# Kernel optimization log

Hardware: AMD Instinct MI355X
Metric: run time of the kernel (lower is better)

Reference implementation:

```python
import jax, jax.numpy as jnp
import numpy as np

B, T, D = 2, 1024, 384
d = D // 3            # 128
D3 = 3 * d            # 384
D9 = 9 * d            # 1152
GAMMA = 5.0
EPS_W = 1e-8
EPS_N = 1e-5


def _orth(rng, n):
    q, _ = np.linalg.qr(rng.standard_normal((n, n)).astype(np.float64))
    return jnp.asarray(q.astype(np.float32))


def setup_inputs() -> dict:
    key = jax.random.key(0)
    x = jax.random.normal(key, (B, T, D), dtype=jnp.float32)
    rng = np.random.default_rng(0)
    def plin(fan_in, fan_out):
        W = jnp.asarray(rng.standard_normal((fan_out, fan_in)).astype(np.float32) * 0.05)
        b = jnp.zeros((fan_out,), jnp.float32)
        return W, b
    Wq, bq = plin(d, D3); Sq = _orth(rng, D3)
    Wk, bk = plin(d, D3); Sk = _orth(rng, D3)
    Wv, bv = plin(d, D3); Sv = _orth(rng, D3)
    Wp, bp = plin(D3, D9)
    gn = jnp.ones((D9,), jnp.float32)
    bn = jnp.zeros((D9,), jnp.float32)
    return {"x": x, "Wq": Wq, "bq": bq, "Sq": Sq, "Wk": Wk, "bk": bk, "Sk": Sk,
            "Wv": Wv, "bv": bv, "Sv": Sv, "Wp": Wp, "bp": bp, "gn": gn, "bn": bn}


def _plin(x, W, b):
    # PositiveLinearHK: linear with softplus-positive weights
    return x @ jax.nn.softplus(W).T + b


def reference(x, Wq, bq, Sq, Wk, bk, Sk, Wv, bv, Sv, Wp, bp, gn, bn):
    Q_base = x[:, :, 0 * d:1 * d]
    K_base = x[:, :, 1 * d:2 * d]
    V_base = x[:, :, 2 * d:3 * d]
    # proj = PositiveLinearHK -> SingleStiefelProjector (orthogonal mixing)
    Q = _plin(Q_base, Wq, bq) @ Sq          # (B,T,3d)
    K = _plin(K_base, Wk, bk) @ Sk
    V = _plin(V_base, Wv, bv) @ Sv
    dots = jnp.einsum('bti,btj->btij', Q, K)            # (B,T,3d,3d)
    scores = jax.nn.sigmoid(GAMMA * dots)
    weights = scores / (scores.sum(axis=-1, keepdims=True) + EPS_W)
    attended = jnp.einsum('btij,btj->bti', weights, V)  # (B,T,3d)
    h = _plin(attended, Wp, bp)                         # (B,T,9d)
    mu = h.mean(axis=-1, keepdims=True)
    var = h.var(axis=-1, keepdims=True)
    return (h - mu) * jax.lax.rsqrt(var + EPS_N) * gn + bn
```

## Files before the change

### kernel.cpp

```cpp
#include <hip/hip_runtime.h>
#include <hip/hip_bf16.h>
#include <math.h>

#define NTOK  2048
#define DD    128
#define DD3   384
#define DD9   1152
#define TB    4
#define GAMMA_F 5.0f
#define LN2_F   0.69314718f
#define LOG2E_F 1.44269504f

#define OFF_M    0
#define OFF_C    147456
#define OFF_WP2  148608

__device__ __forceinline__ float softplusf(float x) {
    return fmaxf(x, 0.0f) + log1pf(__expf(-fabsf(x)));
}
__device__ __forceinline__ unsigned short f2bf(float f) {
    __hip_bfloat16 h = __float2bfloat16(f);
    return *reinterpret_cast<unsigned short*>(&h);
}
__device__ __forceinline__ float exp2_fast(float x) {
#if __has_builtin(__builtin_amdgcn_exp2f)
    return __builtin_amdgcn_exp2f(x);
#else
    return __expf(x * LN2_F);
#endif
}

__global__ __launch_bounds__(384) void k_prep(const float* __restrict__ Wq, const float* __restrict__ Wk,
                                              const float* __restrict__ Wv, const float* __restrict__ Wp,
                                              const float* __restrict__ Sq, const float* __restrict__ Sk,
                                              const float* __restrict__ Sv, const float* __restrict__ bq,
                                              const float* __restrict__ bk, const float* __restrict__ bv,
                                              float* __restrict__ ws) {
    __shared__ float sw[DD3];
    int b = blockIdx.x, tid = threadIdx.x;
    if (b < 384) {
        int idx = b * 384 + tid;
        int i = idx / DD3, m = idx % DD3;
        unsigned d0 = f2bf(softplusf(Wp[(0 * DD3 + m) * DD3 + i]) - LN2_F);
        unsigned d1 = f2bf(softplusf(Wp[(1 * DD3 + m) * DD3 + i]) - LN2_F);
        unsigned d2 = f2bf(softplusf(Wp[(2 * DD3 + m) * DD3 + i]) - LN2_F);
        uint2 u; u.x = d0 | (d1 << 16); u.y = d2;
        ((uint2*)(ws + OFF_WP2))[idx] = u;
    } else if (b < 768) {
        int bb = b - 384;
        int mat = bb >> 7, i = bb & 127;
        const float* W = (mat == 0) ? Wq : (mat == 1 ? Wk : Wv);
        const float* S = (mat == 0) ? Sq : (mat == 1 ? Sk : Sv);
        int m = tid;
        sw[m] = softplusf(W[m * DD + i]);
        __syncthreads();
        const float4* sw4 = (const float4*)sw;
        float a0 = 0.f, a1 = 0.f, a2 = 0.f, a3 = 0.f;
        for (int j4 = 0; j4 < 96; ++j4) {
            float4 w = sw4[j4];
            int j = j4 * 4;
            a0 = fmaf(w.x, S[(j + 0) * DD3 + m], a0);
            a1 = fmaf(w.y, S[(j + 1) * DD3 + m], a1);
            a2 = fmaf(w.z, S[(j + 2) * DD3 + m], a2);
            a3 = fmaf(w.w, S[(j + 3) * DD3 + m], a3);
        }
        ws[OFF_M + mat * 49152 + i * DD3 + m] = (a0 + a1) + (a2 + a3);
    } else {
        int mat = b - 768;
        const float* S = (mat == 0) ? Sq : (mat == 1 ? Sk : Sv);
        const float* bb_ = (mat == 0) ? bq : (mat == 1 ? bk : bv);
        int m = tid;
        float a0 = 0.f, a1 = 0.f, a2 = 0.f, a3 = 0.f;
        for (int j4 = 0; j4 < 96; ++j4) {
            int j = j4 * 4;
            a0 = fmaf(bb_[j + 0], S[(j + 0) * DD3 + m], a0);
            a1 = fmaf(bb_[j + 1], S[(j + 1) * DD3 + m], a1);
            a2 = fmaf(bb_[j + 2], S[(j + 2) * DD3 + m], a2);
            a3 = fmaf(bb_[j + 3], S[(j + 3) * DD3 + m], a3);
        }
        ws[OFF_C + mat * DD3 + m] = (a0 + a1) + (a2 + a3);
    }
}

#define SIGROW(NQ, RS, AV) do {                                        \
        float e0 = exp2_fast((NQ) * kk.x);                             \
        float e1 = exp2_fast((NQ) * kk.y);                             \
        float e2 = exp2_fast((NQ) * kk.z);                             \
        float e3 = exp2_fast((NQ) * kk.w);                             \
        float s0 = __builtin_amdgcn_rcpf(1.0f + e0);                   \
        float s1 = __builtin_amdgcn_rcpf(1.0f + e1);                   \
        float s2 = __builtin_amdgcn_rcpf(1.0f + e2);                   \
        float s3 = __builtin_amdgcn_rcpf(1.0f + e3);                   \
        RS += (s0 + s1) + (s2 + s3);                                   \
        AV = fmaf(s0, vv.x, fmaf(s1, vv.y, fmaf(s2, vv.z, fmaf(s3, vv.w, AV)))); \
    } while (0)

__global__ __launch_bounds__(384, 3) void k_fused(const float* __restrict__ x,
                                                  const float* __restrict__ bp,
                                                  const float* __restrict__ gn,
                                                  const float* __restrict__ bn,
                                                  const float* __restrict__ ws,
                                                  float* __restrict__ out) {
    __shared__ float qkv[3 * TB * DD3];
    __shared__ float att[TB * DD3];
    __shared__ float red[32];
    __shared__ float ssum[TB], smu[TB], sinv[TB];

    int tid = threadIdx.x;
    int tok0 = blockIdx.x * TB;
    const float* xb = x + (size_t)tok0 * DD3;

#pragma unroll
    for (int mat = 0; mat < 3; ++mat) {
        const float* M = ws + OFF_M + mat * 49152;
        const float* xt0 = xb + 0 * DD3 + mat * DD;
        const float* xt1 = xb + 1 * DD3 + mat * DD;
        const float* xt2 = xb + 2 * DD3 + mat * DD;
        const float* xt3 = xb + 3 * DD3 + mat * DD;
        float a0 = 0.f, a1 = 0.f, a2 = 0.f, a3 = 0.f;
        for (int i = 0; i < DD; i += 4) {
            float m0 = M[(i + 0) * DD3 + tid];
            float m1 = M[(i + 1) * DD3 + tid];
            float m2 = M[(i + 2) * DD3 + tid];
            float m3 = M[(i + 3) * DD3 + tid];
            a0 = fmaf(xt0[i], m0, fmaf(xt0[i + 1], m1, fmaf(xt0[i + 2], m2, fmaf(xt0[i + 3], m3, a0))));
            a1 = fmaf(xt1[i], m0, fmaf(xt1[i + 1], m1, fmaf(xt1[i + 2], m2, fmaf(xt1[i + 3], m3, a1))));
            a2 = fmaf(xt2[i], m0, fmaf(xt2[i + 1], m1, fmaf(xt2[i + 2], m2, fmaf(xt2[i + 3], m3, a2))));
            a3 = fmaf(xt3[i], m0, fmaf(xt3[i + 1], m1, fmaf(xt3[i + 2], m2, fmaf(xt3[i + 3], m3, a3))));
        }
        float c = ws[OFF_C + mat * DD3 + tid];
        qkv[(mat * TB + 0) * DD3 + tid] = a0 + c;
        qkv[(mat * TB + 1) * DD3 + tid] = a1 + c;
        qkv[(mat * TB + 2) * DD3 + tid] = a2 + c;
        qkv[(mat * TB + 3) * DD3 + tid] = a3 + c;
    }
    __syncthreads();

    {
        int t  = tid / 96;
        int ts = tid - t * 96;
        const float* Qt = qkv + t * DD3;
        float nq0 = Qt[ts +   0] * (-GAMMA_F * LOG2E_F);
        float nq1 = Qt[ts +  96] * (-GAMMA_F * LOG2E_F);
        float nq2 = Qt[ts + 192] * (-GAMMA_F * LOG2E_F);
        float nq3 = Qt[ts + 288] * (-GAMMA_F * LOG2E_F);
        const float4* K4 = (const float4*)(qkv + (TB + t) * DD3);
        const float4* V4 = (const float4*)(qkv + (2 * TB + t) * DD3);
        float rs0 = 0.f, rs1 = 0.f, rs2 = 0.f, rs3 = 0.f;
        float av0 = 0.f, av1 = 0.f, av2 = 0.f, av3 = 0.f;
        for (int j4 = 0; j4 < 96; ++j4) {
            float4 kk = K4[j4];
            float4 vv = V4[j4];
            SIGROW(nq0, rs0, av0);
            SIGROW(nq1, rs1, av1);
            SIGROW(nq2, rs2, av2);
            SIGROW(nq3, rs3, av3);
        }
        att[t * DD3 + ts +   0] = av0 * __builtin_amdgcn_rcpf(rs0 + 1e-8f);
        att[t * DD3 + ts +  96] = av1 * __builtin_amdgcn_rcpf(rs1 + 1e-8f);
        att[t * DD3 + ts + 192] = av2 * __builtin_amdgcn_rcpf(rs2 + 1e-8f);
        att[t * DD3 + ts + 288] = av3 * __builtin_amdgcn_rcpf(rs3 + 1e-8f);
    }
    __syncthreads();

    int wave = tid >> 6, lane = tid & 63;

    {
        float s0 = att[0 * DD3 + tid];
        float s1 = att[1 * DD3 + tid];
        float s2 = att[2 * DD3 + tid];
        float s3 = att[3 * DD3 + tid];
#pragma unroll
        for (int off = 32; off; off >>= 1) {
            s0 += __shfl_down(s0, off, 64);
            s1 += __shfl_down(s1, off, 64);
            s2 += __shfl_down(s2, off, 64);
            s3 += __shfl_down(s3, off, 64);
        }
        if (lane == 0) {
            red[0 * 8 + wave] = s0; red[1 * 8 + wave] = s1;
            red[2 * 8 + wave] = s2; red[3 * 8 + wave] = s3;
        }
        __syncthreads();
        if (tid < TB) {
            float a = 0.f;
            for (int w = 0; w < 6; ++w) a += red[tid * 8 + w];
            ssum[tid] = a;
        }
        __syncthreads();
    }

    const uint2* wp2 = (const uint2*)(ws + OFF_WP2);
    float acc[3][TB];
    {
        float bp0 = bp[tid], bp1 = bp[tid + DD3], bp2 = bp[tid + 2 * DD3];
#pragma unroll
        for (int t = 0; t < TB; ++t) {
            float base = LN2_F * ssum[t];
            acc[0][t] = bp0 + base;
            acc[1][t] = bp1 + base;
            acc[2][t] = bp2 + base;
        }
    }
    const float4* att4 = (const float4*)att;
    for (int i4 = 0; i4 < 96; ++i4) {
        float4 a0 = att4[0 * 96 + i4];
        float4 a1 = att4[1 * 96 + i4];
        float4 a2 = att4[2 * 96 + i4];
        float4 a3 = att4[3 * 96 + i4];
        const float* af0 = (const float*)&a0;
        const float* af1 = (const float*)&a1;
        const float* af2 = (const float*)&a2;
        const float* af3 = (const float*)&a3;
#pragma unroll
        for (int e = 0; e < 4; ++e) {
            uint2 u = wp2[(i4 * 4 + e) * DD3 + tid];
            float w0 = __uint_as_float(u.x << 16);
            float w1 = __uint_as_float(u.x & 0xffff0000u);
            float w2 = __uint_as_float(u.y << 16);
            acc[0][0] = fmaf(af0[e], w0, acc[0][0]);
            acc[1][0] = fmaf(af0[e], w1, acc[1][0]);
            acc[2][0] = fmaf(af0[e], w2, acc[2][0]);
            acc[0][1] = fmaf(af1[e], w0, acc[0][1]);
            acc[1][1] = fmaf(af1[e], w1, acc[1][1]);
            acc[2][1] = fmaf(af1[e], w2, acc[2][1]);
            acc[0][2] = fmaf(af2[e], w0, acc[0][2]);
            acc[1][2] = fmaf(af2[e], w1, acc[1][2]);
            acc[2][2] = fmaf(af2[e], w2, acc[2][2]);
            acc[0][3] = fmaf(af3[e], w0, acc[0][3]);
            acc[1][3] = fmaf(af3[e], w1, acc[1][3]);
            acc[2][3] = fmaf(af3[e], w2, acc[2][3]);
        }
    }

#pragma unroll
    for (int t = 0; t < TB; ++t) {
        float s = acc[0][t] + acc[1][t] + acc[2][t];
#pragma unroll
        for (int off = 32; off; off >>= 1) s += __shfl_down(s, off, 64);
        if (lane == 0) red[t * 8 + wave] = s;
    }
    __syncthreads();
    if (tid < TB) {
        float a = 0.f;
        for (int w = 0; w < 6; ++w) a += red[tid * 8 + w];
        smu[tid] = a * (1.0f / 1152.0f);
    }
    __syncthreads();
#pragma unroll
    for (int t = 0; t < TB; ++t) {
        float mu = smu[t];
        acc[0][t] -= mu; acc[1][t] -= mu; acc[2][t] -= mu;
        float s = fmaf(acc[0][t], acc[0][t], fmaf(acc[1][t], acc[1][t], acc[2][t] * acc[2][t]));
#pragma unroll
        for (int off = 32; off; off >>= 1) s += __shfl_down(s, off, 64);
        if (lane == 0) red[t * 8 + wave] = s;
    }
    __syncthreads();
    if (tid < TB) {
        float b = 0.f;
        for (int w = 0; w < 6; ++w) b += red[tid * 8 + w];
        sinv[tid] = __builtin_amdgcn_rsqf(b * (1.0f / 1152.0f) + 1e-5f);
    }
    __syncthreads();
    float g0 = gn[tid], g1 = gn[tid + DD3], g2 = gn[tid + 2 * DD3];
    float b0 = bn[tid], b1 = bn[tid + DD3], b2 = bn[tid + 2 * DD3];
#pragma unroll
    for (int t = 0; t < TB; ++t) {
        float inv = sinv[t];
        size_t base = (size_t)(tok0 + t) * DD9;
        out[base + tid]           = fmaf(acc[0][t] * inv, g0, b0);
        out[base + tid + DD3]     = fmaf(acc[1][t] * inv, g1, b1);
        out[base + tid + 2 * DD3] = fmaf(acc[2][t] * inv, g2, b2);
    }
}

extern "C" void kernel_launch(void* const* d_in, const int* in_sizes, int n_in,
                              void* d_out, int out_size, void* d_ws, size_t ws_size,
                              hipStream_t stream) {
    const float* x  = (const float*)d_in[0];
    const float* Wq = (const float*)d_in[1];
    const float* bq = (const float*)d_in[2];
    const float* Sq = (const float*)d_in[3];
    const float* Wk = (const float*)d_in[4];
    const float* bk = (const float*)d_in[5];
    const float* Sk = (const float*)d_in[6];
    const float* Wv = (const float*)d_in[7];
    const float* bv = (const float*)d_in[8];
    const float* Sv = (const float*)d_in[9];
    const float* Wp = (const float*)d_in[10];
    const float* bp = (const float*)d_in[11];
    const float* gn = (const float*)d_in[12];
    const float* bn = (const float*)d_in[13];
    float* out = (float*)d_out;
    float* ws  = (float*)d_ws;

    hipLaunchKernelGGL(k_prep, dim3(771), dim3(384), 0, stream,
                       Wq, Wk, Wv, Wp, Sq, Sk, Sv, bq, bk, bv, ws);
    hipLaunchKernelGGL(k_fused, dim3(NTOK / TB), dim3(384), 0, stream, x, bp, gn, bn, ws, out);
}
```

Before: 159.4 us.

## Halve tokens per block to two, double occupancy, use packed FMA

Cuts tokens per block from four to two, which doubles the grid to 1024 blocks, and raises the launch-bounds occupancy hint from 3 to 6. The attention stage is remapped so each thread handles two query rows instead of four. The output projection now accumulates with 2-wide vector FMAs that can map to packed fp32 FMA. The aim is more blocks to fill the CUs and better latency hiding, at the cost of half the reuse of each projection weight loaded from global memory, so weight traffic doubles.

```diff
diff --git a/kernel.cpp b/kernel.cpp
--- a/kernel.cpp
+++ b/kernel.cpp
@@ -6,7 +6,7 @@
 #define DD    128
 #define DD3   384
 #define DD9   1152
-#define TB    4
+#define TB    2
 #define GAMMA_F 5.0f
 #define LN2_F   0.69314718f
 #define LOG2E_F 1.44269504f
@@ -14,6 +14,8 @@
 #define OFF_M    0
 #define OFF_C    147456
 #define OFF_WP2  148608
+
+typedef __attribute__((ext_vector_type(2))) float f32x2;
 
 __device__ __forceinline__ float softplusf(float x) {
     return fmaxf(x, 0.0f) + log1pf(__expf(-fabsf(x)));
@@ -95,7 +97,7 @@
         AV = fmaf(s0, vv.x, fmaf(s1, vv.y, fmaf(s2, vv.z, fmaf(s3, vv.w, AV)))); \
     } while (0)
 
-__global__ __launch_bounds__(384, 3) void k_fused(const float* __restrict__ x,
+__global__ __launch_bounds__(384, 6) void k_fused(const float* __restrict__ x,
                                                   const float* __restrict__ bp,
                                                   const float* __restrict__ gn,
                                                   const float* __restrict__ bn,
@@ -103,7 +105,7 @@
                                                   float* __restrict__ out) {
     __shared__ float qkv[3 * TB * DD3];
     __shared__ float att[TB * DD3];
-    __shared__ float red[32];
+    __shared__ float red[16];
     __shared__ float ssum[TB], smu[TB], sinv[TB];
 
     int tid = threadIdx.x;
@@ -115,9 +117,7 @@
         const float* M = ws + OFF_M + mat * 49152;
         const float* xt0 = xb + 0 * DD3 + mat * DD;
         const float* xt1 = xb + 1 * DD3 + mat * DD;
-        const float* xt2 = xb + 2 * DD3 + mat * DD;
-        const float* xt3 = xb + 3 * DD3 + mat * DD;
-        float a0 = 0.f, a1 = 0.f, a2 = 0.f, a3 = 0.f;
+        float a0 = 0.f, a1 = 0.f;
         for (int i = 0; i < DD; i += 4) {
             float m0 = M[(i + 0) * DD3 + tid];
             float m1 = M[(i + 1) * DD3 + tid];
@@ -125,62 +125,44 @@
             float m3 = M[(i + 3) * DD3 + tid];
             a0 = fmaf(xt0[i], m0, fmaf(xt0[i + 1], m1, fmaf(xt0[i + 2], m2, fmaf(xt0[i + 3], m3, a0))));
             a1 = fmaf(xt1[i], m0, fmaf(xt1[i + 1], m1, fmaf(xt1[i + 2], m2, fmaf(xt1[i + 3], m3, a1))));
-            a2 = fmaf(xt2[i], m0, fmaf(xt2[i + 1], m1, fmaf(xt2[i + 2], m2, fmaf(xt2[i + 3], m3, a2))));
-            a3 = fmaf(xt3[i], m0, fmaf(xt3[i + 1], m1, fmaf(xt3[i + 2], m2, fmaf(xt3[i + 3], m3, a3))));
         }
         float c = ws[OFF_C + mat * DD3 + tid];
         qkv[(mat * TB + 0) * DD3 + tid] = a0 + c;
         qkv[(mat * TB + 1) * DD3 + tid] = a1 + c;
-        qkv[(mat * TB + 2) * DD3 + tid] = a2 + c;
-        qkv[(mat * TB + 3) * DD3 + tid] = a3 + c;
     }
     __syncthreads();
 
     {
-        int t  = tid / 96;
-        int ts = tid - t * 96;
+        int t  = tid / 192;
+        int ts = tid - t * 192;
         const float* Qt = qkv + t * DD3;
-        float nq0 = Qt[ts +   0] * (-GAMMA_F * LOG2E_F);
-        float nq1 = Qt[ts +  96] * (-GAMMA_F * LOG2E_F);
-        float nq2 = Qt[ts + 192] * (-GAMMA_F * LOG2E_F);
-        float nq3 = Qt[ts + 288] * (-GAMMA_F * LOG2E_F);
+        float nq0 = Qt[ts]       * (-GAMMA_F * LOG2E_F);
+        float nq1 = Qt[ts + 192] * (-GAMMA_F * LOG2E_F);
         const float4* K4 = (const float4*)(qkv + (TB + t) * DD3);
         const float4* V4 = (const float4*)(qkv + (2 * TB + t) * DD3);
-        float rs0 = 0.f, rs1 = 0.f, rs2 = 0.f, rs3 = 0.f;
-        float av0 = 0.f, av1 = 0.f, av2 = 0.f, av3 = 0.f;
+        float rs0 = 0.f, rs1 = 0.f, av0 = 0.f, av1 = 0.f;
         for (int j4 = 0; j4 < 96; ++j4) {
             float4 kk = K4[j4];
             float4 vv = V4[j4];
             SIGROW(nq0, rs0, av0);
             SIGROW(nq1, rs1, av1);
-            SIGROW(nq2, rs2, av2);
-            SIGROW(nq3, rs3, av3);
-        }
-        att[t * DD3 + ts +   0] = av0 * __builtin_amdgcn_rcpf(rs0 + 1e-8f);
-        att[t * DD3 + ts +  96] = av1 * __builtin_amdgcn_rcpf(rs1 + 1e-8f);
-        att[t * DD3 + ts + 192] = av2 * __builtin_amdgcn_rcpf(rs2 + 1e-8f);
-        att[t * DD3 + ts + 288] = av3 * __builtin_amdgcn_rcpf(rs3 + 1e-8f);
-    }
-    __syncthreads();
-
-    int wave = tid >> 6, lane = tid & 63;
+        }
+        att[t * DD3 + ts]       = av0 * __builtin_amdgcn_rcpf(rs0 + 1e-8f);
+        att[t * DD3 + ts + 192] = av1 * __builtin_amdgcn_rcpf(rs1 + 1e-8f);
+    }
+    __syncthreads();
+
+    int wave = tid >> 6, lane64 = tid & 63;
 
     {
         float s0 = att[0 * DD3 + tid];
         float s1 = att[1 * DD3 + tid];
-        float s2 = att[2 * DD3 + tid];
-        float s3 = att[3 * DD3 + tid];
 #pragma unroll
         for (int off = 32; off; off >>= 1) {
             s0 += __shfl_down(s0, off, 64);
             s1 += __shfl_down(s1, off, 64);
-            s2 += __shfl_down(s2, off, 64);
-            s3 += __shfl_down(s3, off, 64);
-        }
-        if (lane == 0) {
-            red[0 * 8 + wave] = s0; red[1 * 8 + wave] = s1;
-            red[2 * 8 + wave] = s2; red[3 * 8 + wave] = s3;
-        }
+        }
+        if (lane64 == 0) { red[wave] = s0; red[8 + wave] = s1; }
         __syncthreads();
         if (tid < TB) {
             float a = 0.f;
@@ -191,54 +173,40 @@
     }
 
     const uint2* wp2 = (const uint2*)(ws + OFF_WP2);
-    float acc[3][TB];
+    f32x2 acc2[3];
     {
         float bp0 = bp[tid], bp1 = bp[tid + DD3], bp2 = bp[tid + 2 * DD3];
-#pragma unroll
-        for (int t = 0; t < TB; ++t) {
-            float base = LN2_F * ssum[t];
-            acc[0][t] = bp0 + base;
-            acc[1][t] = bp1 + base;
-            acc[2][t] = bp2 + base;
-        }
+        float b0 = LN2_F * ssum[0], b1 = LN2_F * ssum[1];
+        acc2[0] = (f32x2){bp0 + b0, bp0 + b1};
+        acc2[1] = (f32x2){bp1 + b0, bp1 + b1};
+        acc2[2] = (f32x2){bp2 + b0, bp2 + b1};
     }
     const float4* att4 = (const float4*)att;
     for (int i4 = 0; i4 < 96; ++i4) {
         float4 a0 = att4[0 * 96 + i4];
         float4 a1 = att4[1 * 96 + i4];
-        float4 a2 = att4[2 * 96 + i4];
-        float4 a3 = att4[3 * 96 + i4];
         const float* af0 = (const float*)&a0;
         const float* af1 = (const float*)&a1;
-        const float* af2 = (const float*)&a2;
-        const float* af3 = (const float*)&a3;
 #pragma unroll
         for (int e = 0; e < 4; ++e) {
             uint2 u = wp2[(i4 * 4 + e) * DD3 + tid];
             float w0 = __uint_as_float(u.x << 16);
             float w1 = __uint_as_float(u.x & 0xffff0000u);
             float w2 = __uint_as_float(u.y << 16);
-            acc[0][0] = fmaf(af0[e], w0, acc[0][0]);
-            acc[1][0] = fmaf(af0[e], w1, acc[1][0]);
-            acc[2][0] = fmaf(af0[e], w2, acc[2][0]);
-            acc[0][1] = fmaf(af1[e], w0, acc[0][1]);
-            acc[1][1] = fmaf(af1[e], w1, acc[1][1]);
-            acc[2][1] = fmaf(af1[e], w2, acc[2][1]);
-            acc[0][2] = fmaf(af2[e], w0, acc[0][2]);
-            acc[1][2] = fmaf(af2[e], w1, acc[1][2]);
-            acc[2][2] = fmaf(af2[e], w2, acc[2][2]);
-            acc[0][3] = fmaf(af3[e], w0, acc[0][3]);
-            acc[1][3] = fmaf(af3[e], w1, acc[1][3]);
-            acc[2][3] = fmaf(af3[e], w2, acc[2][3]);
-        }
-    }
+            f32x2 a01 = (f32x2){af0[e], af1[e]};
+            acc2[0] = __builtin_elementwise_fma(a01, (f32x2){w0, w0}, acc2[0]);
+            acc2[1] = __builtin_elementwise_fma(a01, (f32x2){w1, w1}, acc2[1]);
+            acc2[2] = __builtin_elementwise_fma(a01, (f32x2){w2, w2}, acc2[2]);
+        }
+    }
+    float av_[3][TB] = {{acc2[0].x, acc2[0].y}, {acc2[1].x, acc2[1].y}, {acc2[2].x, acc2[2].y}};
 
 #pragma unroll
     for (int t = 0; t < TB; ++t) {
-        float s = acc[0][t] + acc[1][t] + acc[2][t];
+        float s = av_[0][t] + av_[1][t] + av_[2][t];
 #pragma unroll
         for (int off = 32; off; off >>= 1) s += __shfl_down(s, off, 64);
-        if (lane == 0) red[t * 8 + wave] = s;
+        if (lane64 == 0) red[t * 8 + wave] = s;
     }
     __syncthreads();
     if (tid < TB) {
@@ -250,11 +218,11 @@
 #pragma unroll
     for (int t = 0; t < TB; ++t) {
         float mu = smu[t];
-        acc[0][t] -= mu; acc[1][t] -= mu; acc[2][t] -= mu;
-        float s = fmaf(acc[0][t], acc[0][t], fmaf(acc[1][t], acc[1][t], acc[2][t] * acc[2][t]));
+        av_[0][t] -= mu; av_[1][t] -= mu; av_[2][t] -= mu;
+        float s = fmaf(av_[0][t], av_[0][t], fmaf(av_[1][t], av_[1][t], av_[2][t] * av_[2][t]));
 #pragma unroll
         for (int off = 32; off; off >>= 1) s += __shfl_down(s, off, 64);
-        if (lane == 0) red[t * 8 + wave] = s;
+        if (lane64 == 0) red[t * 8 + wave] = s;
     }
     __syncthreads();
     if (tid < TB) {
@@ -269,9 +237,9 @@
     for (int t = 0; t < TB; ++t) {
         float inv = sinv[t];
         size_t base = (size_t)(tok0 + t) * DD9;
-        out[base + tid]           = fmaf(acc[0][t] * inv, g0, b0);
-        out[base + tid + DD3]     = fmaf(acc[1][t] * inv, g1, b1);
-        out[base + tid + 2 * DD3] = fmaf(acc[2][t] * inv, g2, b2);
+        out[base + tid]           = fmaf(av_[0][t] * inv, g0, b0);
+        out[base + tid + DD3]     = fmaf(av_[1][t] * inv, g1, b1);
+        out[base + tid + 2 * DD3] = fmaf(av_[2][t] * inv, g2, b2);
     }
 }
 
```

Result: faster. 155.5 us (-2.4%).
